# Kernel optimization log

Measured on AMD Instinct MI355X. Metric: run time of the kernel, lower is better.

Reference implementation:

```python
import jax, jax.numpy as jnp
import numpy as np

N_NODES = 50000
N_EDGES = 1600000
NUM_BASIS = 10
HIDDEN = 64
MAX_RADIUS = 3.0
WEIGHT_NUMEL = 5  # paths: (0x0->0),(0x1->1),(1x0->1),(1x1->0),(1x1->1)


def setup_inputs() -> dict:
    key = jax.random.key(0)
    k1, k2, k3, k4, k5 = jax.random.split(key, 5)
    f_1 = jax.random.normal(k1, (N_NODES, 4), dtype=jnp.float32)
    pos = jax.random.uniform(k2, (N_NODES, 3), dtype=jnp.float32) * MAX_RADIUS
    edge_index = jax.random.randint(k3, (2, N_EDGES), 0, N_NODES, dtype=jnp.int64)
    # radial MLP params (e3nn FullyConnectedNet init: std-normal weights)
    W1 = jax.random.normal(k4, (NUM_BASIS, HIDDEN), dtype=jnp.float32)
    W2 = jax.random.normal(k5, (HIDDEN, WEIGHT_NUMEL), dtype=jnp.float32)
    return {"f_1": f_1, "pos": pos, "W1": W1, "W2": W2, "edge_index": edge_index}


def _forward(f_1, pos, W1, W2, edge_index):
    row, col = edge_index[0], edge_index[1]
    num_nodes = f_1.shape[0]
    num_neighbors = edge_index.shape[1] / num_nodes

    edge_vec = pos[row] - pos[col]                      # [E,3]
    r2 = jnp.sum(edge_vec * edge_vec, axis=-1)
    r = jnp.sqrt(jnp.maximum(r2, 1e-12))                # [E]
    unit = edge_vec / r[:, None]

    # spherical harmonics 0e+1e, component normalization, e3nn (y,z,x) order
    sh = jnp.concatenate(
        [jnp.ones_like(unit[:, :1]), jnp.sqrt(3.0) * unit[:, [1, 2, 0]]], axis=-1
    )                                                   # [E,4]

    # soft_one_hot_linspace, basis='smooth_finite', cutoff=True
    values = jnp.linspace(0.0, MAX_RADIUS, NUM_BASIS + 2)[1:-1]
    step = values[1] - values[0]
    diff = (r[:, None] - values) / step                 # [E,num_basis]
    inside = jnp.abs(diff) < 1.0
    d = jnp.where(inside, diff, 0.0)
    C = 1.14136 * float(np.e) ** 2
    emb = jnp.where(inside, C * jnp.exp(-1.0 / (1.0 + d) - 1.0 / (1.0 - d)), 0.0)

    # e3nn FullyConnectedNet [num_basis, hidden, weight_numel] with relu
    # hidden: act normalized to unit 2nd moment (relu -> *sqrt(2)); weights /sqrt(fan_in)
    h = jax.nn.relu(emb @ (W1 / jnp.sqrt(float(NUM_BASIS)))) * jnp.sqrt(2.0)
    w = h @ (W2 / jnp.sqrt(float(HIDDEN)))              # [E,5]

    # FullyConnectedTensorProduct (0e+1e) x (0e+1e) -> (0e+1e), per-edge weights
    x = f_1[row]
    x0, xv = x[:, 0], x[:, 1:4]
    y0, yv = sh[:, 0], sh[:, 1:4]
    inv_s3 = 1.0 / jnp.sqrt(3.0)
    inv_s6 = 1.0 / jnp.sqrt(6.0)
    # output 0e: fan-in 2 paths -> norm sqrt(1/2)
    out0 = jnp.sqrt(0.5) * (
        w[:, 0] * x0 * y0 + w[:, 3] * jnp.sum(xv * yv, axis=-1) * inv_s3
    )
    # output 1e: fan-in 3 paths -> norm sqrt(3/3)=1
    outv = (
        w[:, 1:2] * x0[:, None] * yv * inv_s3
        + w[:, 2:3] * xv * y0[:, None] * inv_s3
        + w[:, 4:5] * jnp.cross(xv, yv) * inv_s6
    )
    f_edge = jnp.concatenate([out0[:, None], outv], axis=-1)  # [E,4]

    out = jax.ops.segment_sum(f_edge, col, num_segments=num_nodes)
    return out / jnp.sqrt(num_neighbors).astype(out.dtype)


def reference(f_1, pos, W1, W2, edge_index):
    return _forward(f_1, pos, W1, W2, edge_index)
```

## Files before the change

### kernel.cpp

```cpp
#include <hip/hip_runtime.h>
#include <math.h>

#define N_NODES_C 50000
#define N_EDGES_C 1600000
#define EPB 1024
#define NBLK_E 1563
#define NBUCKET 256
#define NB_USED 196
#define NCHUNK 6
#define CHUNK_B 261
#define TBL 256

#define QSCALE 1024.0f
#define QINV   (1.0f / 1024.0f)

__device__ __forceinline__ int detect_is64_block(const void* eidx, int t, int* lds_flag) {
    if (t < 64) {
        const long long* p = (const long long*)eidx;
        bool ok = true;
        for (int k = 0; k < 4; ++k) {
            long long v = p[t * 4 + k];
            ok &= (v >= 0 && v < (long long)N_NODES_C);
        }
        unsigned long long m = __ballot(ok);
        if (t == 0) *lds_flag = (m == ~0ull) ? 1 : 0;
    }
    __syncthreads();
    return *lds_flag;
}

__device__ __forceinline__ int load_col(const void* eidx, int is64, int e) {
    return is64 ? (int)((const long long*)eidx)[N_EDGES_C + e]
                : ((const int*)eidx)[N_EDGES_C + e];
}
__device__ __forceinline__ int load_row(const void* eidx, int is64, int e) {
    return is64 ? (int)((const long long*)eidx)[e]
                : ((const int*)eidx)[e];
}

__device__ __forceinline__ void edge_quant(const float* __restrict__ f1,
                                           const float* __restrict__ pos,
                                           const float* __restrict__ w1s,
                                           const float* __restrict__ W2,
                                           int row, int col, int v[4]) {
    v[0] = v[1] = v[2] = v[3] = 0;
    float px = pos[row * 3 + 0] - pos[col * 3 + 0];
    float py = pos[row * 3 + 1] - pos[col * 3 + 1];
    float pz = pos[row * 3 + 2] - pos[col * 3 + 2];
    float r2 = px * px + py * py + pz * pz;
    float r = sqrtf(fmaxf(r2, 1e-12f));
    float inv_r = 1.0f / r;
    float ux = px * inv_r, uy = py * inv_r, uz = pz * inv_r;
    const float SQ3 = 1.7320508075688772f;
    float yv0 = SQ3 * uy, yv1 = SQ3 * uz, yv2 = SQ3 * ux;

    const float C = 8.433573069075486f;
    float tt = r * (11.0f / 3.0f);
    int k1 = (int)tt;
    float d = tt - (float)k1;
    float e0 = 0.f, e1 = 0.f;
    int b0 = 0, b1 = 0;
    if (k1 >= 1 && k1 <= 10) {
        b0 = k1 - 1;
        e0 = C * __expf(-1.0f / (1.0f + d) - 1.0f / (1.0f - d));
    }
    int k2 = k1 + 1;
    if (k2 <= 10 && d > 0.f) {
        b1 = k2 - 1;
        float d2 = d - 1.0f;
        e1 = C * __expf(-1.0f / (1.0f + d2) - 1.0f / (1.0f - d2));
    }
    if (e0 == 0.f && e1 == 0.f) return;

    const float* r0 = &w1s[b0 * 68];
    const float* r1 = &w1s[b1 * 68];
    float w0 = 0.f, w1a = 0.f, w2a = 0.f, w3 = 0.f, w4 = 0.f;
#pragma unroll
    for (int j = 0; j < 64; j += 4) {
        float4 a = *(const float4*)(r0 + j);
        float4 b = *(const float4*)(r1 + j);
        float h0 = fmaxf(e0 * a.x + e1 * b.x, 0.f);
        float h1 = fmaxf(e0 * a.y + e1 * b.y, 0.f);
        float h2 = fmaxf(e0 * a.z + e1 * b.z, 0.f);
        float h3 = fmaxf(e0 * a.w + e1 * b.w, 0.f);
        w0  += h0 * W2[(j + 0) * 5 + 0] + h1 * W2[(j + 1) * 5 + 0] + h2 * W2[(j + 2) * 5 + 0] + h3 * W2[(j + 3) * 5 + 0];
        w1a += h0 * W2[(j + 0) * 5 + 1] + h1 * W2[(j + 1) * 5 + 1] + h2 * W2[(j + 2) * 5 + 1] + h3 * W2[(j + 3) * 5 + 1];
        w2a += h0 * W2[(j + 0) * 5 + 2] + h1 * W2[(j + 1) * 5 + 2] + h2 * W2[(j + 2) * 5 + 2] + h3 * W2[(j + 3) * 5 + 2];
        w3  += h0 * W2[(j + 0) * 5 + 3] + h1 * W2[(j + 1) * 5 + 3] + h2 * W2[(j + 2) * 5 + 3] + h3 * W2[(j + 3) * 5 + 3];
        w4  += h0 * W2[(j + 0) * 5 + 4] + h1 * W2[(j + 1) * 5 + 4] + h2 * W2[(j + 2) * 5 + 4] + h3 * W2[(j + 3) * 5 + 4];
    }
    const float SC = 0.05590169943749474f;
    w0 *= SC; w1a *= SC; w2a *= SC; w3 *= SC; w4 *= SC;

    float4 x = *(const float4*)(f1 + row * 4);
    float x0 = x.x, xv0 = x.y, xv1 = x.z, xv2 = x.w;

    const float INV_S3 = 0.5773502691896258f;
    const float INV_S6 = 0.4082482904638631f;
    const float SQH    = 0.7071067811865476f;
    const float INV_SQRT_NN = 0.17677669529663687f;

    float dotxy = xv0 * yv0 + xv1 * yv1 + xv2 * yv2;
    float out0 = SQH * (w0 * x0 + w3 * dotxy * INV_S3) * INV_SQRT_NN;
    float cx0 = xv1 * yv2 - xv2 * yv1;
    float cx1 = xv2 * yv0 - xv0 * yv2;
    float cx2 = xv0 * yv1 - xv1 * yv0;
    float o1 = (w1a * x0 * yv0 * INV_S3 + w2a * xv0 * INV_S3 + w4 * cx0 * INV_S6) * INV_SQRT_NN;
    float o2 = (w1a * x0 * yv1 * INV_S3 + w2a * xv1 * INV_S3 + w4 * cx1 * INV_S6) * INV_SQRT_NN;
    float o3 = (w1a * x0 * yv2 * INV_S3 + w2a * xv2 * INV_S3 + w4 * cx2 * INV_S6) * INV_SQRT_NN;

    v[0] = min(8191, max(-8191, (int)rintf(out0 * QSCALE)));
    v[1] = min(8191, max(-8191, (int)rintf(o1   * QSCALE)));
    v[2] = min(8191, max(-8191, (int)rintf(o2   * QSCALE)));
    v[3] = min(8191, max(-8191, (int)rintf(o3   * QSCALE)));
}

__global__ __launch_bounds__(256)
void scatter2_kernel(const float* __restrict__ f1, const float* __restrict__ pos,
                     const float* __restrict__ W1, const float* __restrict__ W2,
                     const void* __restrict__ eidx,
                     unsigned long long* __restrict__ scratchP,
                     unsigned short* __restrict__ starts) {
    __shared__ float w1s[10 * 68];
    __shared__ float tC0[TBL];
    __shared__ float tC1[TBL];
    __shared__ float tC2[TBL];
    __shared__ float tC3[TBL];
    __shared__ float tC4[TBL];
    __shared__ unsigned hist[NBUCKET];
    __shared__ unsigned pfx[NBUCKET];
    __shared__ unsigned cursor[NBUCKET];
    __shared__ unsigned stageLo[EPB];
    __shared__ unsigned stageHi[EPB];
    __shared__ unsigned short colbuf[EPB];
    __shared__ int flag_s;
    const int t = threadIdx.x;
    for (int i = t; i < 640; i += 256) w1s[(i >> 6) * 68 + (i & 63)] = W1[i];
    hist[t] = 0u;
    const int is64 = detect_is64_block(eidx, t, &flag_s);

    {
        float tt = (float)t * (11.0f / 255.0f);
        int k1 = (int)tt;
        float d = tt - (float)k1;
        const float C = 8.433573069075486f;
        float e0 = 0.f, e1 = 0.f;
        int b0 = 0, b1 = 0;
        if (k1 >= 1 && k1 <= 10) {
            b0 = k1 - 1;
            e0 = C * __expf(-1.0f / (1.0f + d) - 1.0f / (1.0f - d));
        }
        int k2 = k1 + 1;
        if (k2 <= 10 && d > 0.f) {
            b1 = k2 - 1;
            float d2 = d - 1.0f;
            e1 = C * __expf(-1.0f / (1.0f + d2) - 1.0f / (1.0f - d2));
        }
        float w0 = 0.f, w1 = 0.f, w2 = 0.f, w3 = 0.f, w4 = 0.f;
        const float* r0 = &w1s[b0 * 68];
        const float* r1 = &w1s[b1 * 68];
#pragma unroll
        for (int j = 0; j < 64; j += 4) {
            float4 a = *(const float4*)(r0 + j);
            float4 b = *(const float4*)(r1 + j);
            float h0 = fmaxf(e0 * a.x + e1 * b.x, 0.f);
            float h1 = fmaxf(e0 * a.y + e1 * b.y, 0.f);
            float h2 = fmaxf(e0 * a.z + e1 * b.z, 0.f);
            float h3 = fmaxf(e0 * a.w + e1 * b.w, 0.f);
            w0 += h0 * W2[(j + 0) * 5 + 0] + h1 * W2[(j + 1) * 5 + 0] + h2 * W2[(j + 2) * 5 + 0] + h3 * W2[(j + 3) * 5 + 0];
            w1 += h0 * W2[(j + 0) * 5 + 1] + h1 * W2[(j + 1) * 5 + 1] + h2 * W2[(j + 2) * 5 + 1] + h3 * W2[(j + 3) * 5 + 1];
            w2 += h0 * W2[(j + 0) * 5 + 2] + h1 * W2[(j + 1) * 5 + 2] + h2 * W2[(j + 2) * 5 + 2] + h3 * W2[(j + 3) * 5 + 2];
            w3 += h0 * W2[(j + 0) * 5 + 3] + h1 * W2[(j + 1) * 5 + 3] + h2 * W2[(j + 2) * 5 + 3] + h3 * W2[(j + 3) * 5 + 3];
            w4 += h0 * W2[(j + 0) * 5 + 4] + h1 * W2[(j + 1) * 5 + 4] + h2 * W2[(j + 2) * 5 + 4] + h3 * W2[(j + 3) * 5 + 4];
        }
        const float SC  = 0.05590169943749474f;
        const float ISN = 0.17677669529663687f;
        const float SQH = 0.7071067811865476f;
        const float INV_S3 = 0.5773502691896258f;
        const float INV_S6 = 0.4082482904638631f;
        const float SQ3 = 1.7320508075688772f;
        float base = SC * ISN;
        tC0[t] = SQH * base * w0;
        tC1[t] = base * w1;
        tC2[t] = INV_S3 * base * w2;
        tC3[t] = SQH * base * w3;
        tC4[t] = INV_S6 * SQ3 * base * w4;
    }

    const int e0b = blockIdx.x * EPB;
    for (int i = t; i < EPB; i += 256) {
        int e = e0b + i;
        if (e < N_EDGES_C) {
            int col = load_col(eidx, is64, e);
            colbuf[i] = (unsigned short)col;
            atomicAdd(&hist[col >> 8], 1u);
        }
    }
    __syncthreads();
    pfx[t] = hist[t];
    __syncthreads();
    for (int off = 1; off < 256; off <<= 1) {
        unsigned x = (t >= off) ? pfx[t - off] : 0u;
        __syncthreads();
        pfx[t] += x;
        __syncthreads();
    }
    unsigned excl = pfx[t] - hist[t];
    cursor[t] = excl;
    starts[blockIdx.x * 257 + t] = (unsigned short)excl;
    if (t == 255) starts[blockIdx.x * 257 + 256] = (unsigned short)pfx[255];
    __syncthreads();
    for (int i = t; i < EPB; i += 256) {
        int e = e0b + i;
        if (e >= N_EDGES_C) continue;
        int row = load_row(eidx, is64, e);
        int col = (int)colbuf[i];

        float px = pos[row * 3 + 0] - pos[col * 3 + 0];
        float py = pos[row * 3 + 1] - pos[col * 3 + 1];
        float pz = pos[row * 3 + 2] - pos[col * 3 + 2];
        float r2 = px * px + py * py + pz * pz;
        float r = sqrtf(fmaxf(r2, 1e-12f));
        float inv_r = 1.0f / r;
        float uv0 = py * inv_r, uv1 = pz * inv_r, uv2 = px * inv_r;

        float ft = fminf(r * (255.0f / 3.0f), 255.0f);
        int idx = min((int)ft, TBL - 2);
        float fr = ft - (float)idx;
        float c0 = fmaf(fr, tC0[idx + 1] - tC0[idx], tC0[idx]);
        float c1 = fmaf(fr, tC1[idx + 1] - tC1[idx], tC1[idx]);
        float c2 = fmaf(fr, tC2[idx + 1] - tC2[idx], tC2[idx]);
        float c3 = fmaf(fr, tC3[idx + 1] - tC3[idx], tC3[idx]);
        float c4 = fmaf(fr, tC4[idx + 1] - tC4[idx], tC4[idx]);

        float4 x = *(const float4*)(f1 + row * 4);
        float x0 = x.x, xv0 = x.y, xv1 = x.z, xv2 = x.w;

        float dotxy = xv0 * uv0 + xv1 * uv1 + xv2 * uv2;
        float out0 = c0 * x0 + c3 * dotxy;
        float cx0 = xv1 * uv2 - xv2 * uv1;
        float cx1 = xv2 * uv0 - xv0 * uv2;
        float cx2 = xv0 * uv1 - xv1 * uv0;
        float c1x = c1 * x0;
        float o1 = c1x * uv0 + c2 * xv0 + c4 * cx0;
        float o2 = c1x * uv1 + c2 * xv1 + c4 * cx1;
        float o3 = c1x * uv2 + c2 * xv2 + c4 * cx2;

        int v0 = min(8191, max(-8191, (int)rintf(out0 * QSCALE)));
        int v1 = min(8191, max(-8191, (int)rintf(o1 * QSCALE)));
        int v2 = min(8191, max(-8191, (int)rintf(o2 * QSCALE)));
        int v3 = min(8191, max(-8191, (int)rintf(o3 * QSCALE)));

        unsigned long long P = ((unsigned long long)(unsigned)(col & 255) << 56)
                             | ((unsigned long long)(unsigned)(v3 & 0x3FFF) << 42)
                             | ((unsigned long long)(unsigned)(v2 & 0x3FFF) << 28)
                             | ((unsigned long long)(unsigned)(v1 & 0x3FFF) << 14)
                             | ((unsigned long long)(unsigned)(v0 & 0x3FFF));
        unsigned p = atomicAdd(&cursor[col >> 8], 1u);
        stageLo[p] = (unsigned)P;
        stageHi[p] = (unsigned)(P >> 32);
    }
    __syncthreads();
    const int total = (int)pfx[255];
    unsigned long long* dst = scratchP + (size_t)blockIdx.x * EPB;
    for (int i = t; i < total; i += 256) {
        dst[i] = ((unsigned long long)stageHi[i] << 32) | (unsigned long long)stageLo[i];
    }
}

__global__ __launch_bounds__(256)
void gather2_kernel(const unsigned long long* __restrict__ scratchP,
                    const unsigned short* __restrict__ starts,
                    unsigned long long* __restrict__ partials) {
    __shared__ unsigned long long accs[NBUCKET];
    const int t = threadIdx.x;
    const int k = blockIdx.x;
    const int c = blockIdx.y;
    accs[t] = 0ull;
    __syncthreads();
    const int b_lo = c * CHUNK_B;
    const int b_hi = (c == NCHUNK - 1) ? NBLK_E : (b_lo + CHUNK_B);
    for (int b = b_lo + t; b < b_hi; b += 256) {
        int s = starts[b * 257 + k];
        int e = starts[b * 257 + k + 1];
        const unsigned long long* src = scratchP + (size_t)b * EPB;
        for (int i = s; i < e; ++i) {
            unsigned long long P = src[i];
            long long sp = (long long)P;
            long long v0 = (sp << 50) >> 50;
            long long v1 = (sp << 36) >> 50;
            long long v2 = (sp << 22) >> 50;
            long long v3 = (sp << 8)  >> 50;
            int col8 = (int)(P >> 56);
            unsigned long long Q = (unsigned long long)(v0 + (v1 << 16) + (v2 << 32) + (v3 << 48));
            atomicAdd(&accs[col8], Q);
        }
    }
    __syncthreads();
    int node = (k << 8) + t;
    if (node < N_NODES_C) partials[(size_t)c * N_NODES_C + node] = accs[t];
}

__global__ __launch_bounds__(256)
void reduce3_kernel(const unsigned long long* __restrict__ partials, float* __restrict__ out) {
    int n = blockIdx.x * 256 + threadIdx.x;
    if (n >= N_NODES_C) return;
    unsigned long long s = 0ull;
#pragma unroll
    for (int c = 0; c < NCHUNK; ++c) s += partials[(size_t)c * N_NODES_C + n];
    long long T = (long long)s;
    int s0 = (int)(short)(T & 0xFFFF); T = (T - s0) >> 16;
    int s1 = (int)(short)(T & 0xFFFF); T = (T - s1) >> 16;
    int s2 = (int)(short)(T & 0xFFFF); T = (T - s2) >> 16;
    int s3 = (int)T;
    float4 o;
    o.x = (float)s0 * QINV;
    o.y = (float)s1 * QINV;
    o.z = (float)s2 * QINV;
    o.w = (float)s3 * QINV;
    *(float4*)(out + 4 * n) = o;
}

__global__ __launch_bounds__(256)
void init_acc(unsigned long long* __restrict__ acc,
              const void* __restrict__ eidx, int* __restrict__ flag) {
    int i = blockIdx.x * 256 + threadIdx.x;
    if (i < N_NODES_C) acc[i] = 0ull;
    if (blockIdx.x == 0 && threadIdx.x < 64) {
        const long long* p = (const long long*)eidx;
        bool ok = true;
        for (int k = 0; k < 4; ++k) {
            long long v = p[threadIdx.x * 4 + k];
            ok &= (v >= 0 && v < (long long)N_NODES_C);
        }
        unsigned long long m = __ballot(ok);
        if (threadIdx.x == 0) *flag = (m == ~0ull) ? 1 : 0;
    }
}

__global__ __launch_bounds__(256)
void reduce_unpack(const unsigned long long* __restrict__ acc, float* __restrict__ out) {
    int n = blockIdx.x * 256 + threadIdx.x;
    if (n >= N_NODES_C) return;
    long long T = (long long)acc[n];
    int s0 = (int)(short)(T & 0xFFFF); T = (T - s0) >> 16;
    int s1 = (int)(short)(T & 0xFFFF); T = (T - s1) >> 16;
    int s2 = (int)(short)(T & 0xFFFF); T = (T - s2) >> 16;
    int s3 = (int)T;
    float4 o;
    o.x = (float)s0 * QINV; o.y = (float)s1 * QINV;
    o.z = (float)s2 * QINV; o.w = (float)s3 * QINV;
    *(float4*)(out + 4 * n) = o;
}

__global__ __launch_bounds__(256)
void equi_conv_atomic(const float* __restrict__ f1, const float* __restrict__ pos,
                      const float* __restrict__ W1, const float* __restrict__ W2,
                      const void* __restrict__ eidx, const int* __restrict__ flag_p,
                      unsigned long long* __restrict__ acc) {
    __shared__ float w1s[10 * 68];
    const int tid = threadIdx.x;
    for (int i = tid; i < 640; i += 256) w1s[(i >> 6) * 68 + (i & 63)] = W1[i];
    __syncthreads();
    const int e = blockIdx.x * 256 + tid;
    if (e >= N_EDGES_C) return;
    const int is64 = *flag_p;
    int row = load_row(eidx, is64, e);
    int col = load_col(eidx, is64, e);
    int v[4];
    edge_quant(f1, pos, w1s, W2, row, col, v);
    if (v[0] | v[1] | v[2] | v[3]) {
        unsigned long long P = (unsigned long long)((long long)v[0] + ((long long)v[1] << 16)
                             + ((long long)v[2] << 32) + ((long long)v[3] << 48));
        __hip_atomic_fetch_add(acc + col, P, __ATOMIC_RELAXED, __HIP_MEMORY_SCOPE_AGENT);
    }
}

extern "C" void kernel_launch(void* const* d_in, const int* in_sizes, int n_in,
                              void* d_out, int out_size, void* d_ws, size_t ws_size,
                              hipStream_t stream) {
    const float* f1  = (const float*)d_in[0];
    const float* pos = (const float*)d_in[1];
    const float* W1  = (const float*)d_in[2];
    const float* W2  = (const float*)d_in[3];
    const void*  eix = d_in[4];
    float* out = (float*)d_out;

    const size_t offP = 0;
    const size_t szP  = (size_t)NBLK_E * EPB * 8;
    const size_t offS = offP + szP;
    const size_t szS  = (size_t)NBLK_E * 257 * 2;
    const size_t offR = (offS + szS + 7) & ~(size_t)7;
    const size_t szR  = (size_t)NCHUNK * N_NODES_C * 8;
    const size_t need_sort = offR + szR;

    if (ws_size >= need_sort) {
        unsigned long long* scratchP = (unsigned long long*)((char*)d_ws + offP);
        unsigned short*     starts   = (unsigned short*)((char*)d_ws + offS);
        unsigned long long* partials = (unsigned long long*)((char*)d_ws + offR);

        scatter2_kernel<<<NBLK_E, 256, 0, stream>>>(f1, pos, W1, W2, eix, scratchP, starts);
        gather2_kernel<<<dim3(NB_USED, NCHUNK), 256, 0, stream>>>(scratchP, starts, partials);
        reduce3_kernel<<<NB_USED, 256, 0, stream>>>(partials, out);
    } else {
        unsigned long long* acc = (unsigned long long*)d_ws;
        int* flag = (int*)((char*)d_ws + (size_t)N_NODES_C * 8);
        const int nblk = (N_NODES_C + 255) / 256;
        init_acc<<<nblk, 256, 0, stream>>>(acc, eix, flag);
        equi_conv_atomic<<<(N_EDGES_C + 255) / 256, 256, 0, stream>>>(f1, pos, W1, W2, eix, flag, acc);
        reduce_unpack<<<nblk, 256, 0, stream>>>(acc, out);
    }
}
```

Measured before the change: 125.8 us.

## Bucket edges into global per-bucket regions via atomic cursors and pack node data

```diff
diff --git a/kernel.cpp b/kernel.cpp
--- a/kernel.cpp
+++ b/kernel.cpp
@@ -7,9 +7,9 @@
 #define NBLK_E 1563
 #define NBUCKET 256
 #define NB_USED 196
-#define NCHUNK 6
-#define CHUNK_B 261
+#define NCH2 8
 #define TBL 256
+#define CAPLOG 16
 
 #define QSCALE 1024.0f
 #define QINV   (1.0f / 1024.0f)
@@ -116,11 +116,29 @@
 }
 
 __global__ __launch_bounds__(256)
-void scatter2_kernel(const float* __restrict__ f1, const float* __restrict__ pos,
+void prep_kernel(const float* __restrict__ pos, const float* __restrict__ f1,
+                 float* __restrict__ nodeq, unsigned* __restrict__ gCursor) {
+    const int t = threadIdx.x;
+    if (blockIdx.x == 0) gCursor[t] = (unsigned)t << CAPLOG;
+    int n = blockIdx.x * 256 + t;
+    if (n < N_NODES_C) {
+        float4 f = *(const float4*)(f1 + 4 * n);
+        float4 p;
+        p.x = pos[3 * n + 0];
+        p.y = pos[3 * n + 1];
+        p.z = pos[3 * n + 2];
+        p.w = 0.f;
+        *(float4*)(nodeq + 8 * n)     = p;
+        *(float4*)(nodeq + 8 * n + 4) = f;
+    }
+}
+
+__global__ __launch_bounds__(256)
+void scatter3_kernel(const float* __restrict__ nodeq,
                      const float* __restrict__ W1, const float* __restrict__ W2,
                      const void* __restrict__ eidx,
-                     unsigned long long* __restrict__ scratchP,
-                     unsigned short* __restrict__ starts) {
+                     unsigned* __restrict__ gCursor,
+                     unsigned long long* __restrict__ scratchG) {
     __shared__ float w1s[10 * 68];
     __shared__ float tC0[TBL];
     __shared__ float tC1[TBL];
@@ -128,10 +146,7 @@
     __shared__ float tC3[TBL];
     __shared__ float tC4[TBL];
     __shared__ unsigned hist[NBUCKET];
-    __shared__ unsigned pfx[NBUCKET];
     __shared__ unsigned cursor[NBUCKET];
-    __shared__ unsigned stageLo[EPB];
-    __shared__ unsigned stageHi[EPB];
     __shared__ unsigned short colbuf[EPB];
     __shared__ int flag_s;
     const int t = threadIdx.x;
@@ -197,18 +212,10 @@
         }
     }
     __syncthreads();
-    pfx[t] = hist[t];
-    __syncthreads();
-    for (int off = 1; off < 256; off <<= 1) {
-        unsigned x = (t >= off) ? pfx[t - off] : 0u;
-        __syncthreads();
-        pfx[t] += x;
-        __syncthreads();
-    }
-    unsigned excl = pfx[t] - hist[t];
-    cursor[t] = excl;
-    starts[blockIdx.x * 257 + t] = (unsigned short)excl;
-    if (t == 255) starts[blockIdx.x * 257 + 256] = (unsigned short)pfx[255];
+    {
+        unsigned h = hist[t];
+        cursor[t] = h ? atomicAdd(&gCursor[t], h) : 0u;
+    }
     __syncthreads();
     for (int i = t; i < EPB; i += 256) {
         int e = e0b + i;
@@ -216,9 +223,15 @@
         int row = load_row(eidx, is64, e);
         int col = (int)colbuf[i];
 
-        float px = pos[row * 3 + 0] - pos[col * 3 + 0];
-        float py = pos[row * 3 + 1] - pos[col * 3 + 1];
-        float pz = pos[row * 3 + 2] - pos[col * 3 + 2];
+        const float* nr = nodeq + ((size_t)row << 3);
+        const float* nc = nodeq + ((size_t)col << 3);
+        float4 pr = *(const float4*)nr;
+        float4 xx = *(const float4*)(nr + 4);
+        float4 pc = *(const float4*)nc;
+
+        float px = pr.x - pc.x;
+        float py = pr.y - pc.y;
+        float pz = pr.z - pc.z;
         float r2 = px * px + py * py + pz * pz;
         float r = sqrtf(fmaxf(r2, 1e-12f));
         float inv_r = 1.0f / r;
@@ -233,8 +246,7 @@
         float c3 = fmaf(fr, tC3[idx + 1] - tC3[idx], tC3[idx]);
         float c4 = fmaf(fr, tC4[idx + 1] - tC4[idx], tC4[idx]);
 
-        float4 x = *(const float4*)(f1 + row * 4);
-        float x0 = x.x, xv0 = x.y, xv1 = x.z, xv2 = x.w;
+        float x0 = xx.x, xv0 = xx.y, xv1 = xx.z, xv2 = xx.w;
 
         float dotxy = xv0 * uv0 + xv1 * uv1 + xv2 * uv2;
         float out0 = c0 * x0 + c3 * dotxy;
@@ -256,21 +268,15 @@
                              | ((unsigned long long)(unsigned)(v2 & 0x3FFF) << 28)
                              | ((unsigned long long)(unsigned)(v1 & 0x3FFF) << 14)
                              | ((unsigned long long)(unsigned)(v0 & 0x3FFF));
-        unsigned p = atomicAdd(&cursor[col >> 8], 1u);
-        stageLo[p] = (unsigned)P;
-        stageHi[p] = (unsigned)(P >> 32);
-    }
-    __syncthreads();
-    const int total = (int)pfx[255];
-    unsigned long long* dst = scratchP + (size_t)blockIdx.x * EPB;
-    for (int i = t; i < total; i += 256) {
-        dst[i] = ((unsigned long long)stageHi[i] << 32) | (unsigned long long)stageLo[i];
-    }
-}
-
-__global__ __launch_bounds__(256)
-void gather2_kernel(const unsigned long long* __restrict__ scratchP,
-                    const unsigned short* __restrict__ starts,
+        int bucket = col >> 8;
+        unsigned p = atomicAdd(&cursor[bucket], 1u);
+        if (p < ((unsigned)(bucket + 1) << CAPLOG)) scratchG[p] = P;
+    }
+}
+
+__global__ __launch_bounds__(256)
+void gather3_kernel(const unsigned long long* __restrict__ scratchG,
+                    const unsigned* __restrict__ gCursor,
                     unsigned long long* __restrict__ partials) {
     __shared__ unsigned long long accs[NBUCKET];
     const int t = threadIdx.x;
@@ -278,23 +284,21 @@
     const int c = blockIdx.y;
     accs[t] = 0ull;
     __syncthreads();
-    const int b_lo = c * CHUNK_B;
-    const int b_hi = (c == NCHUNK - 1) ? NBLK_E : (b_lo + CHUNK_B);
-    for (int b = b_lo + t; b < b_hi; b += 256) {
-        int s = starts[b * 257 + k];
-        int e = starts[b * 257 + k + 1];
-        const unsigned long long* src = scratchP + (size_t)b * EPB;
-        for (int i = s; i < e; ++i) {
-            unsigned long long P = src[i];
-            long long sp = (long long)P;
-            long long v0 = (sp << 50) >> 50;
-            long long v1 = (sp << 36) >> 50;
-            long long v2 = (sp << 22) >> 50;
-            long long v3 = (sp << 8)  >> 50;
-            int col8 = (int)(P >> 56);
-            unsigned long long Q = (unsigned long long)(v0 + (v1 << 16) + (v2 << 32) + (v3 << 48));
-            atomicAdd(&accs[col8], Q);
-        }
+    unsigned cnt = gCursor[k] - ((unsigned)k << CAPLOG);
+    cnt = min(cnt, (unsigned)(1u << CAPLOG));
+    unsigned i0 = (unsigned)(((unsigned long long)cnt * (unsigned)c) / NCH2);
+    unsigned i1 = (unsigned)(((unsigned long long)cnt * (unsigned)(c + 1)) / NCH2);
+    const unsigned long long* src = scratchG + ((size_t)k << CAPLOG);
+    for (unsigned i = i0 + t; i < i1; i += 256) {
+        unsigned long long P = src[i];
+        long long sp = (long long)P;
+        long long v0 = (sp << 50) >> 50;
+        long long v1 = (sp << 36) >> 50;
+        long long v2 = (sp << 22) >> 50;
+        long long v3 = (sp << 8)  >> 50;
+        int col8 = (int)(P >> 56);
+        unsigned long long Q = (unsigned long long)(v0 + (v1 << 16) + (v2 << 32) + (v3 << 48));
+        atomicAdd(&accs[col8], Q);
     }
     __syncthreads();
     int node = (k << 8) + t;
@@ -307,7 +311,7 @@
     if (n >= N_NODES_C) return;
     unsigned long long s = 0ull;
 #pragma unroll
-    for (int c = 0; c < NCHUNK; ++c) s += partials[(size_t)c * N_NODES_C + n];
+    for (int c = 0; c < NCH2; ++c) s += partials[(size_t)c * N_NODES_C + n];
     long long T = (long long)s;
     int s0 = (int)(short)(T & 0xFFFF); T = (T - s0) >> 16;
     int s1 = (int)(short)(T & 0xFFFF); T = (T - s1) >> 16;
@@ -386,21 +390,25 @@
     const void*  eix = d_in[4];
     float* out = (float*)d_out;
 
-    const size_t offP = 0;
-    const size_t szP  = (size_t)NBLK_E * EPB * 8;
-    const size_t offS = offP + szP;
-    const size_t szS  = (size_t)NBLK_E * 257 * 2;
-    const size_t offR = (offS + szS + 7) & ~(size_t)7;
-    const size_t szR  = (size_t)NCHUNK * N_NODES_C * 8;
+    const size_t offG = 0;
+    const size_t szG  = (size_t)NBUCKET << CAPLOG << 3;
+    const size_t offC = offG + szG;
+    const size_t szC  = (size_t)NBUCKET * 4;
+    const size_t offQ = (offC + szC + 15) & ~(size_t)15;
+    const size_t szQ  = (size_t)N_NODES_C * 32;
+    const size_t offR = (offQ + szQ + 7) & ~(size_t)7;
+    const size_t szR  = (size_t)NCH2 * N_NODES_C * 8;
     const size_t need_sort = offR + szR;
 
     if (ws_size >= need_sort) {
-        unsigned long long* scratchP = (unsigned long long*)((char*)d_ws + offP);
-        unsigned short*     starts   = (unsigned short*)((char*)d_ws + offS);
+        unsigned long long* scratchG = (unsigned long long*)((char*)d_ws + offG);
+        unsigned*           gCursor  = (unsigned*)((char*)d_ws + offC);
+        float*              nodeq    = (float*)((char*)d_ws + offQ);
         unsigned long long* partials = (unsigned long long*)((char*)d_ws + offR);
 
-        scatter2_kernel<<<NBLK_E, 256, 0, stream>>>(f1, pos, W1, W2, eix, scratchP, starts);
-        gather2_kernel<<<dim3(NB_USED, NCHUNK), 256, 0, stream>>>(scratchP, starts, partials);
+        prep_kernel<<<NB_USED, 256, 0, stream>>>(pos, f1, nodeq, gCursor);
+        scatter3_kernel<<<NBLK_E, 256, 0, stream>>>(nodeq, W1, W2, eix, gCursor, scratchG);
+        gather3_kernel<<<dim3(NB_USED, NCH2), 256, 0, stream>>>(scratchG, gCursor, partials);
         reduce3_kernel<<<NB_USED, 256, 0, stream>>>(partials, out);
     } else {
         unsigned long long* acc = (unsigned long long*)d_ws;
```

Measured after the change: 131.5 us. 4.5% more time.

## Replace per-block bucket sort with unsorted packets and filtered mega-bucket gather

Applied to the files above, without the earlier changes.

```diff
diff --git a/kernel.cpp b/kernel.cpp
--- a/kernel.cpp
+++ b/kernel.cpp
@@ -5,11 +5,13 @@
 #define N_EDGES_C 1600000
 #define EPB 1024
 #define NBLK_E 1563
-#define NBUCKET 256
-#define NB_USED 196
-#define NCHUNK 6
-#define CHUNK_B 261
+#define NBLK_N 196
 #define TBL 256
+
+#define NMEGA_USED 13
+#define MEGA_NODES 4096
+#define NCH2 64
+#define CHUNK2 (N_EDGES_C / NCH2)
 
 #define QSCALE 1024.0f
 #define QINV   (1.0f / 1024.0f)
@@ -115,28 +117,67 @@
     v[3] = min(8191, max(-8191, (int)rintf(o3   * QSCALE)));
 }
 
-__global__ __launch_bounds__(256)
-void scatter2_kernel(const float* __restrict__ f1, const float* __restrict__ pos,
+__device__ __forceinline__ unsigned long long edge_packet(
+        float prx, float pry, float prz, float4 xx,
+        float pcx, float pcy, float pcz,
+        const float* tC0, const float* tC1, const float* tC2,
+        const float* tC3, const float* tC4, int col) {
+    float px = prx - pcx;
+    float py = pry - pcy;
+    float pz = prz - pcz;
+    float r2 = px * px + py * py + pz * pz;
+    float r = sqrtf(fmaxf(r2, 1e-12f));
+    float inv_r = 1.0f / r;
+    float uv0 = py * inv_r, uv1 = pz * inv_r, uv2 = px * inv_r;
+
+    float ft = fminf(r * (255.0f / 3.0f), 255.0f);
+    int idx = min((int)ft, TBL - 2);
+    float fr = ft - (float)idx;
+    float c0 = fmaf(fr, tC0[idx + 1] - tC0[idx], tC0[idx]);
+    float c1 = fmaf(fr, tC1[idx + 1] - tC1[idx], tC1[idx]);
+    float c2 = fmaf(fr, tC2[idx + 1] - tC2[idx], tC2[idx]);
+    float c3 = fmaf(fr, tC3[idx + 1] - tC3[idx], tC3[idx]);
+    float c4 = fmaf(fr, tC4[idx + 1] - tC4[idx], tC4[idx]);
+
+    float x0 = xx.x, xv0 = xx.y, xv1 = xx.z, xv2 = xx.w;
+
+    float dotxy = xv0 * uv0 + xv1 * uv1 + xv2 * uv2;
+    float out0 = c0 * x0 + c3 * dotxy;
+    float cx0 = xv1 * uv2 - xv2 * uv1;
+    float cx1 = xv2 * uv0 - xv0 * uv2;
+    float cx2 = xv0 * uv1 - xv1 * uv0;
+    float c1x = c1 * x0;
+    float o1 = c1x * uv0 + c2 * xv0 + c4 * cx0;
+    float o2 = c1x * uv1 + c2 * xv1 + c4 * cx1;
+    float o3 = c1x * uv2 + c2 * xv2 + c4 * cx2;
+
+    int v0 = min(8191, max(-8191, (int)rintf(out0 * QSCALE)));
+    int v1 = min(8191, max(-8191, (int)rintf(o1 * QSCALE)));
+    int v2 = min(8191, max(-8191, (int)rintf(o2 * QSCALE)));
+    int v3 = min(8191, max(-8191, (int)rintf(o3 * QSCALE)));
+
+    return ((unsigned long long)(unsigned)(col & 255) << 56)
+         | ((unsigned long long)(unsigned)(v3 & 0x3FFF) << 42)
+         | ((unsigned long long)(unsigned)(v2 & 0x3FFF) << 28)
+         | ((unsigned long long)(unsigned)(v1 & 0x3FFF) << 14)
+         | ((unsigned long long)(unsigned)(v0 & 0x3FFF));
+}
+
+__global__ __launch_bounds__(256)
+void ecompute_kernel(const float* __restrict__ f1, const float* __restrict__ pos,
                      const float* __restrict__ W1, const float* __restrict__ W2,
                      const void* __restrict__ eidx,
                      unsigned long long* __restrict__ scratchP,
-                     unsigned short* __restrict__ starts) {
-    __shared__ float w1s[10 * 68];
+                     unsigned short* __restrict__ colLo) {
     __shared__ float tC0[TBL];
     __shared__ float tC1[TBL];
     __shared__ float tC2[TBL];
     __shared__ float tC3[TBL];
     __shared__ float tC4[TBL];
-    __shared__ unsigned hist[NBUCKET];
-    __shared__ unsigned pfx[NBUCKET];
-    __shared__ unsigned cursor[NBUCKET];
-    __shared__ unsigned stageLo[EPB];
-    __shared__ unsigned stageHi[EPB];
-    __shared__ unsigned short colbuf[EPB];
+    __shared__ float w1s[10 * 68];
     __shared__ int flag_s;
     const int t = threadIdx.x;
     for (int i = t; i < 640; i += 256) w1s[(i >> 6) * 68 + (i & 63)] = W1[i];
-    hist[t] = 0u;
     const int is64 = detect_is64_block(eidx, t, &flag_s);
 
     {
@@ -186,128 +227,105 @@
         tC3[t] = SQH * base * w3;
         tC4[t] = INV_S6 * SQ3 * base * w4;
     }
+    __syncthreads();
 
     const int e0b = blockIdx.x * EPB;
-    for (int i = t; i < EPB; i += 256) {
-        int e = e0b + i;
-        if (e < N_EDGES_C) {
-            int col = load_col(eidx, is64, e);
-            colbuf[i] = (unsigned short)col;
-            atomicAdd(&hist[col >> 8], 1u);
-        }
-    }
+    if (e0b + EPB <= N_EDGES_C) {
+        int e0 = e0b + t, e1 = e0 + 256, e2 = e0 + 512, e3 = e0 + 768;
+        int r0i = load_row(eidx, is64, e0), c0i = load_col(eidx, is64, e0);
+        int r1i = load_row(eidx, is64, e1), c1i = load_col(eidx, is64, e1);
+        int r2i = load_row(eidx, is64, e2), c2i = load_col(eidx, is64, e2);
+        int r3i = load_row(eidx, is64, e3), c3i = load_col(eidx, is64, e3);
+
+        float pr0x = pos[r0i*3+0], pr0y = pos[r0i*3+1], pr0z = pos[r0i*3+2];
+        float pc0x = pos[c0i*3+0], pc0y = pos[c0i*3+1], pc0z = pos[c0i*3+2];
+        float4 xx0 = *(const float4*)(f1 + r0i*4);
+        float pr1x = pos[r1i*3+0], pr1y = pos[r1i*3+1], pr1z = pos[r1i*3+2];
+        float pc1x = pos[c1i*3+0], pc1y = pos[c1i*3+1], pc1z = pos[c1i*3+2];
+        float4 xx1 = *(const float4*)(f1 + r1i*4);
+        float pr2x = pos[r2i*3+0], pr2y = pos[r2i*3+1], pr2z = pos[r2i*3+2];
+        float pc2x = pos[c2i*3+0], pc2y = pos[c2i*3+1], pc2z = pos[c2i*3+2];
+        float4 xx2 = *(const float4*)(f1 + r2i*4);
+        float pr3x = pos[r3i*3+0], pr3y = pos[r3i*3+1], pr3z = pos[r3i*3+2];
+        float pc3x = pos[c3i*3+0], pc3y = pos[c3i*3+1], pc3z = pos[c3i*3+2];
+        float4 xx3 = *(const float4*)(f1 + r3i*4);
+
+        scratchP[e0] = edge_packet(pr0x,pr0y,pr0z,xx0,pc0x,pc0y,pc0z,tC0,tC1,tC2,tC3,tC4,c0i);
+        scratchP[e1] = edge_packet(pr1x,pr1y,pr1z,xx1,pc1x,pc1y,pc1z,tC0,tC1,tC2,tC3,tC4,c1i);
+        scratchP[e2] = edge_packet(pr2x,pr2y,pr2z,xx2,pc2x,pc2y,pc2z,tC0,tC1,tC2,tC3,tC4,c2i);
+        scratchP[e3] = edge_packet(pr3x,pr3y,pr3z,xx3,pc3x,pc3y,pc3z,tC0,tC1,tC2,tC3,tC4,c3i);
+        colLo[e0] = (unsigned short)c0i;
+        colLo[e1] = (unsigned short)c1i;
+        colLo[e2] = (unsigned short)c2i;
+        colLo[e3] = (unsigned short)c3i;
+    } else {
+        for (int i = t; i < N_EDGES_C - e0b; i += 256) {
+            int e = e0b + i;
+            int ri = load_row(eidx, is64, e), ci = load_col(eidx, is64, e);
+            float prx = pos[ri*3+0], pry = pos[ri*3+1], prz = pos[ri*3+2];
+            float pcx = pos[ci*3+0], pcy = pos[ci*3+1], pcz = pos[ci*3+2];
+            float4 xx = *(const float4*)(f1 + ri*4);
+            scratchP[e] = edge_packet(prx,pry,prz,xx,pcx,pcy,pcz,tC0,tC1,tC2,tC3,tC4,ci);
+            colLo[e] = (unsigned short)ci;
+        }
+    }
+}
+
+__device__ __forceinline__ void fg_hit(unsigned cv, int e, unsigned B,
+                                       const unsigned long long* __restrict__ scratchP,
+                                       unsigned long long* accs) {
+    if ((cv >> 12) == B) {
+        unsigned long long P = scratchP[e];
+        long long sp = (long long)P;
+        long long v0 = (sp << 50) >> 50;
+        long long v1 = (sp << 36) >> 50;
+        long long v2 = (sp << 22) >> 50;
+        long long v3 = (sp << 8)  >> 50;
+        unsigned long long Q = (unsigned long long)(v0 + (v1 << 16) + (v2 << 32) + (v3 << 48));
+        atomicAdd(&accs[cv & (MEGA_NODES - 1)], Q);
+    }
+}
+
+__global__ __launch_bounds__(256)
+void fgather_kernel(const unsigned long long* __restrict__ scratchP,
+                    const unsigned short* __restrict__ colLo,
+                    unsigned long long* __restrict__ partials) {
+    __shared__ unsigned long long accs[MEGA_NODES];
+    const int t = threadIdx.x;
+    const unsigned B = blockIdx.x;
+    const int c = blockIdx.y;
+    for (int j = t; j < MEGA_NODES; j += 256) accs[j] = 0ull;
     __syncthreads();
-    pfx[t] = hist[t];
+    const int ebase = c * CHUNK2;
+    const uint4* src = (const uint4*)(colLo + ebase);
+    const int nvec = CHUNK2 / 8;
+    for (int i = t; i < nvec; i += 256) {
+        uint4 v = src[i];
+        int e0 = ebase + i * 8;
+        fg_hit(v.x & 0xFFFFu, e0 + 0, B, scratchP, accs);
+        fg_hit(v.x >> 16,     e0 + 1, B, scratchP, accs);
+        fg_hit(v.y & 0xFFFFu, e0 + 2, B, scratchP, accs);
+        fg_hit(v.y >> 16,     e0 + 3, B, scratchP, accs);
+        fg_hit(v.z & 0xFFFFu, e0 + 4, B, scratchP, accs);
+        fg_hit(v.z >> 16,     e0 + 5, B, scratchP, accs);
+        fg_hit(v.w & 0xFFFFu, e0 + 6, B, scratchP, accs);
+        fg_hit(v.w >> 16,     e0 + 7, B, scratchP, accs);
+    }
     __syncthreads();
-    for (int off = 1; off < 256; off <<= 1) {
-        unsigned x = (t >= off) ? pfx[t - off] : 0u;
-        __syncthreads();
-        pfx[t] += x;
-        __syncthreads();
-    }
-    unsigned excl = pfx[t] - hist[t];
-    cursor[t] = excl;
-    starts[blockIdx.x * 257 + t] = (unsigned short)excl;
-    if (t == 255) starts[blockIdx.x * 257 + 256] = (unsigned short)pfx[255];
-    __syncthreads();
-    for (int i = t; i < EPB; i += 256) {
-        int e = e0b + i;
-        if (e >= N_EDGES_C) continue;
-        int row = load_row(eidx, is64, e);
-        int col = (int)colbuf[i];
-
-        float px = pos[row * 3 + 0] - pos[col * 3 + 0];
-        float py = pos[row * 3 + 1] - pos[col * 3 + 1];
-        float pz = pos[row * 3 + 2] - pos[col * 3 + 2];
-        float r2 = px * px + py * py + pz * pz;
-        float r = sqrtf(fmaxf(r2, 1e-12f));
-        float inv_r = 1.0f / r;
-        float uv0 = py * inv_r, uv1 = pz * inv_r, uv2 = px * inv_r;
-
-        float ft = fminf(r * (255.0f / 3.0f), 255.0f);
-        int idx = min((int)ft, TBL - 2);
-        float fr = ft - (float)idx;
-        float c0 = fmaf(fr, tC0[idx + 1] - tC0[idx], tC0[idx]);
-        float c1 = fmaf(fr, tC1[idx + 1] - tC1[idx], tC1[idx]);
-        float c2 = fmaf(fr, tC2[idx + 1] - tC2[idx], tC2[idx]);
-        float c3 = fmaf(fr, tC3[idx + 1] - tC3[idx], tC3[idx]);
-        float c4 = fmaf(fr, tC4[idx + 1] - tC4[idx], tC4[idx]);
-
-        float4 x = *(const float4*)(f1 + row * 4);
-        float x0 = x.x, xv0 = x.y, xv1 = x.z, xv2 = x.w;
-
-        float dotxy = xv0 * uv0 + xv1 * uv1 + xv2 * uv2;
-        float out0 = c0 * x0 + c3 * dotxy;
-        float cx0 = xv1 * uv2 - xv2 * uv1;
-        float cx1 = xv2 * uv0 - xv0 * uv2;
-        float cx2 = xv0 * uv1 - xv1 * uv0;
-        float c1x = c1 * x0;
-        float o1 = c1x * uv0 + c2 * xv0 + c4 * cx0;
-        float o2 = c1x * uv1 + c2 * xv1 + c4 * cx1;
-        float o3 = c1x * uv2 + c2 * xv2 + c4 * cx2;
-
-        int v0 = min(8191, max(-8191, (int)rintf(out0 * QSCALE)));
-        int v1 = min(8191, max(-8191, (int)rintf(o1 * QSCALE)));
-        int v2 = min(8191, max(-8191, (int)rintf(o2 * QSCALE)));
-        int v3 = min(8191, max(-8191, (int)rintf(o3 * QSCALE)));
-
-        unsigned long long P = ((unsigned long long)(unsigned)(col & 255) << 56)
-                             | ((unsigned long long)(unsigned)(v3 & 0x3FFF) << 42)
-                             | ((unsigned long long)(unsigned)(v2 & 0x3FFF) << 28)
-                             | ((unsigned long long)(unsigned)(v1 & 0x3FFF) << 14)
-                             | ((unsigned long long)(unsigned)(v0 & 0x3FFF));
-        unsigned p = atomicAdd(&cursor[col >> 8], 1u);
-        stageLo[p] = (unsigned)P;
-        stageHi[p] = (unsigned)(P >> 32);
-    }
-    __syncthreads();
-    const int total = (int)pfx[255];
-    unsigned long long* dst = scratchP + (size_t)blockIdx.x * EPB;
-    for (int i = t; i < total; i += 256) {
-        dst[i] = ((unsigned long long)stageHi[i] << 32) | (unsigned long long)stageLo[i];
-    }
-}
-
-__global__ __launch_bounds__(256)
-void gather2_kernel(const unsigned long long* __restrict__ scratchP,
-                    const unsigned short* __restrict__ starts,
-                    unsigned long long* __restrict__ partials) {
-    __shared__ unsigned long long accs[NBUCKET];
-    const int t = threadIdx.x;
-    const int k = blockIdx.x;
-    const int c = blockIdx.y;
-    accs[t] = 0ull;
-    __syncthreads();
-    const int b_lo = c * CHUNK_B;
-    const int b_hi = (c == NCHUNK - 1) ? NBLK_E : (b_lo + CHUNK_B);
-    for (int b = b_lo + t; b < b_hi; b += 256) {
-        int s = starts[b * 257 + k];
-        int e = starts[b * 257 + k + 1];
-        const unsigned long long* src = scratchP + (size_t)b * EPB;
-        for (int i = s; i < e; ++i) {
-            unsigned long long P = src[i];
-            long long sp = (long long)P;
-            long long v0 = (sp << 50) >> 50;
-            long long v1 = (sp << 36) >> 50;
-            long long v2 = (sp << 22) >> 50;
-            long long v3 = (sp << 8)  >> 50;
-            int col8 = (int)(P >> 56);
-            unsigned long long Q = (unsigned long long)(v0 + (v1 << 16) + (v2 << 32) + (v3 << 48));
-            atomicAdd(&accs[col8], Q);
-        }
-    }
-    __syncthreads();
-    int node = (k << 8) + t;
-    if (node < N_NODES_C) partials[(size_t)c * N_NODES_C + node] = accs[t];
-}
-
-__global__ __launch_bounds__(256)
-void reduce3_kernel(const unsigned long long* __restrict__ partials, float* __restrict__ out) {
+    unsigned long long* dst = partials + (((size_t)(B * NCH2 + c)) << 12);
+    for (int j = t; j < MEGA_NODES; j += 256) dst[j] = accs[j];
+}
+
+__global__ __launch_bounds__(256)
+void reduce5_kernel(const unsigned long long* __restrict__ partials, float* __restrict__ out) {
     int n = blockIdx.x * 256 + threadIdx.x;
     if (n >= N_NODES_C) return;
+    int B = n >> 12;
+    int local = n & (MEGA_NODES - 1);
+    const unsigned long long* src = partials + (((size_t)(B * NCH2)) << 12) + local;
     unsigned long long s = 0ull;
 #pragma unroll
-    for (int c = 0; c < NCHUNK; ++c) s += partials[(size_t)c * N_NODES_C + n];
+    for (int c = 0; c < NCH2; ++c) s += src[(size_t)c << 12];
     long long T = (long long)s;
     int s0 = (int)(short)(T & 0xFFFF); T = (T - s0) >> 16;
     int s1 = (int)(short)(T & 0xFFFF); T = (T - s1) >> 16;
@@ -387,21 +405,21 @@
     float* out = (float*)d_out;
 
     const size_t offP = 0;
-    const size_t szP  = (size_t)NBLK_E * EPB * 8;
-    const size_t offS = offP + szP;
-    const size_t szS  = (size_t)NBLK_E * 257 * 2;
-    const size_t offR = (offS + szS + 7) & ~(size_t)7;
-    const size_t szR  = (size_t)NCHUNK * N_NODES_C * 8;
-    const size_t need_sort = offR + szR;
-
-    if (ws_size >= need_sort) {
+    const size_t szP  = (size_t)N_EDGES_C * 8;
+    const size_t offL = (offP + szP + 15) & ~(size_t)15;
+    const size_t szL  = (size_t)N_EDGES_C * 2;
+    const size_t offR = (offL + szL + 15) & ~(size_t)15;
+    const size_t szR  = ((size_t)NMEGA_USED * NCH2) << 12 << 3;
+    const size_t need = offR + szR;
+
+    if (ws_size >= need) {
         unsigned long long* scratchP = (unsigned long long*)((char*)d_ws + offP);
-        unsigned short*     starts   = (unsigned short*)((char*)d_ws + offS);
+        unsigned short*     colLo    = (unsigned short*)((char*)d_ws + offL);
         unsigned long long* partials = (unsigned long long*)((char*)d_ws + offR);
 
-        scatter2_kernel<<<NBLK_E, 256, 0, stream>>>(f1, pos, W1, W2, eix, scratchP, starts);
-        gather2_kernel<<<dim3(NB_USED, NCHUNK), 256, 0, stream>>>(scratchP, starts, partials);
-        reduce3_kernel<<<NB_USED, 256, 0, stream>>>(partials, out);
+        ecompute_kernel<<<NBLK_E, 256, 0, stream>>>(f1, pos, W1, W2, eix, scratchP, colLo);
+        fgather_kernel<<<dim3(NMEGA_USED, NCH2), 256, 0, stream>>>(scratchP, colLo, partials);
+        reduce5_kernel<<<NBLK_N, 256, 0, stream>>>(partials, out);
     } else {
         unsigned long long* acc = (unsigned long long*)d_ws;
         int* flag = (int*)((char*)d_ws + (size_t)N_NODES_C * 8);
```

After: 153.4 us. +21.9%, slower.
